# Performance work log

Hardware: AMD Instinct MI355X
Metric: run time of the kernel (lower is better)

Reference implementation:

```python
import jax, jax.numpy as jnp
import numpy as np

B, C, IH, IW = 16, 512, 28, 28
HEADS, DIM_HEAD = 8, 32
INNER = HEADS * DIM_HEAD            # 256
HIDDEN = 4 * C                      # 2048
N = IH * IW                         # 784 tokens
EPS = 1e-5


def _relative_index(ih, iw):
    coords = np.stack(np.meshgrid(np.arange(ih), np.arange(iw), indexing='ij')).reshape(2, -1)
    rel = coords[:, :, None] - coords[:, None, :]
    rel[0] += ih - 1
    rel[1] += iw - 1
    rel[0] *= 2 * iw - 1
    return jnp.asarray((rel[0] + rel[1]).reshape(-1))  # (n*n,)

REL_IDX = _relative_index(IH, IW)


def _layernorm(x, g, b):
    mu = jnp.mean(x, axis=-1, keepdims=True)
    var = jnp.mean(jnp.square(x - mu), axis=-1, keepdims=True)
    return (x - mu) * jax.lax.rsqrt(var + EPS) * g + b


def setup_inputs() -> dict:
    key = jax.random.key(0)
    ks = jax.random.split(key, 12)
    s = lambda fan_in: 1.0 / np.sqrt(fan_in)
    return {
        'x': jax.random.normal(ks[0], (B, C, IH, IW), jnp.float32),
        'ln1_g': jnp.ones((C,), jnp.float32),
        'ln1_b': jnp.zeros((C,), jnp.float32),
        'qkv_w': jax.random.normal(ks[1], (C, 3 * INNER), jnp.float32) * s(C),
        'qkv_b': jnp.zeros((3 * INNER,), jnp.float32),
        'out_w': jax.random.normal(ks[2], (INNER, C), jnp.float32) * s(INNER),
        'out_b': jnp.zeros((C,), jnp.float32),
        'rel_table': jax.random.normal(ks[3], ((2 * IH - 1) * (2 * IW - 1), HEADS), jnp.float32) * 0.02,
        'ln2_g': jnp.ones((C,), jnp.float32),
        'ln2_b': jnp.zeros((C,), jnp.float32),
        'ff_w1': jax.random.normal(ks[4], (C, HIDDEN), jnp.float32) * s(C),
        'ff_b1': jnp.zeros((HIDDEN,), jnp.float32),
        'ff_w2': jax.random.normal(ks[5], (HIDDEN, C), jnp.float32) * s(HIDDEN),
        'ff_b2': jnp.zeros((C,), jnp.float32),
    }


def reference(x, ln1_g, ln1_b, qkv_w, qkv_b, out_w, out_b, rel_table,
              ln2_g, ln2_b, ff_w1, ff_b1, ff_w2, ff_b2):
    scale = DIM_HEAD ** -0.5
    # b c h w -> b n c
    xs = x.reshape(B, C, N).transpose(0, 2, 1)

    # --- PreNorm attention branch ---
    h = _layernorm(xs, ln1_g, ln1_b)
    qkv = h @ qkv_w + qkv_b                               # [B, N, 3*INNER]
    q, k, v = jnp.split(qkv, 3, axis=-1)
    split_heads = lambda t: t.reshape(B, N, HEADS, DIM_HEAD).transpose(0, 2, 1, 3)
    q, k, v = map(split_heads, (q, k, v))                 # [B, H, N, d]
    dots = jnp.einsum('bhnd,bhmd->bhnm', q, k) * scale    # [B, H, N, N]
    bias = rel_table[REL_IDX].reshape(N, N, HEADS).transpose(2, 0, 1)  # [H, N, N]
    attn = jax.nn.softmax(dots + bias[None], axis=-1)
    o = jnp.einsum('bhnm,bhmd->bhnd', attn, v)            # [B, H, N, d]
    o = o.transpose(0, 2, 1, 3).reshape(B, N, INNER)
    o = o @ out_w + out_b                                 # [B, N, C]
    xs = xs + o                                           # residual

    # --- PreNorm FFN branch ---
    h = _layernorm(xs, ln2_g, ln2_b)
    h = jax.nn.gelu(h @ ff_w1 + ff_b1, approximate=False)
    h = h @ ff_w2 + ff_b2
    xs = xs + h

    # b n c -> b c h w
    return xs.transpose(0, 2, 1).reshape(B, C, IH, IW)
```

## Files before the change

kernel.cpp:

```cpp
#include <hip/hip_runtime.h>
#include <hip/hip_bf16.h>

#define DEVI __device__ __forceinline__

typedef __attribute__((ext_vector_type(8))) short bf16x8;
typedef __attribute__((ext_vector_type(4))) float f32x4;
typedef __attribute__((ext_vector_type(4))) unsigned u32x4;

static constexpr int BB = 16, CC = 512, NT = 784, HD = 8, DH = 32;
static constexpr int INNER = 256, HID = 2048, MTOT = BB * NT;

DEVI short f2bf(float x) {
  unsigned u = __builtin_bit_cast(unsigned, x);
  u += 0x7fffu + ((u >> 16) & 1u);
  return (short)(u >> 16);
}

DEVI void gll16(const void* g, void* l) {
  __builtin_amdgcn_global_load_lds(
      (const __attribute__((address_space(1))) unsigned int*)g,
      (__attribute__((address_space(3))) unsigned int*)l, 16, 0, 0);
}

__device__ void wprep_body(const float* __restrict__ W, short* __restrict__ WT,
                           int K0, int N0, int bx, int by, float* smem) {
  float (*tile)[33] = (float(*)[33])smem;
  const int tk0 = bx * 32, tn0 = by * 32;
  const int tx = threadIdx.x & 31, ty = threadIdx.x >> 5;
#pragma unroll
  for (int i = 0; i < 4; ++i)
    tile[ty + i * 8][tx] = W[(size_t)(tk0 + ty + i * 8) * N0 + tn0 + tx];
  __syncthreads();
#pragma unroll
  for (int i = 0; i < 4; ++i)
    WT[(size_t)(tn0 + ty + i * 8) * K0 + tk0 + tx] = f2bf(tile[tx][ty + i * 8]);
}

__global__ void prep_kernel(const float* __restrict__ qkv_w, short* __restrict__ wqkvT,
                            const float* __restrict__ out_w, short* __restrict__ woutT,
                            const float* __restrict__ ff_w1, short* __restrict__ wf1T,
                            const float* __restrict__ ff_w2, short* __restrict__ wf2T,
                            const float* __restrict__ x, float* __restrict__ xs,
                            const float* __restrict__ rel, short* __restrict__ bt) {
  __shared__ float smem[64 * 17];
  const int bid = blockIdx.x;
  if (bid < 384) {
    wprep_body(qkv_w, wqkvT, 512, 768, bid & 15, bid >> 4, smem);
  } else if (bid < 512) {
    int l = bid - 384;
    wprep_body(out_w, woutT, 256, 512, l & 7, l >> 3, smem);
  } else if (bid < 1536) {
    int l = bid - 512;
    wprep_body(ff_w1, wf1T, 512, 2048, l & 15, l >> 4, smem);
  } else if (bid < 2560) {
    int l = bid - 1536;
    wprep_body(ff_w2, wf2T, 2048, 512, l & 63, l >> 6, smem);
  } else if (bid < 8832) {
    int l = bid - 2560;
    float (*tile)[17] = (float(*)[17])smem;
    const int n0 = (l % 49) * 16, c0 = ((l / 49) & 7) * 64, b = l / 392;
    const int tx = threadIdx.x & 15, ty = threadIdx.x >> 4;
    const float* p = x + ((size_t)b * CC + c0) * NT + n0;
#pragma unroll
    for (int i = 0; i < 4; ++i)
      tile[ty + i * 16][tx] = p[(size_t)(ty + i * 16) * NT + tx];
    __syncthreads();
    float* qd = xs + ((size_t)b * NT + n0) * CC + c0;
    const int cx = threadIdx.x & 63, ny = threadIdx.x >> 6;
#pragma unroll
    for (int i = 0; i < 4; ++i)
      qd[(size_t)(ny + i * 4) * CC + cx] = tile[cx][ny + i * 4];
  } else {
    int id = (bid - 8832) * 256 + threadIdx.x;
    int r = id & 3;
    int mr = (id >> 2) & 1;
    int lane = (id >> 3) & 63;
    int wid = (id >> 9) & 3;
    int t = id >> 11;
    int jhi = t % 49;
    int t2 = t / 49;
    int qc = t2 % 7;
    int h = t2 / 7;
    int i = qc * 128 + wid * 32 + mr * 16 + (lane >> 4) * 4 + r;
    if (i > 783) i = 783;
    int j = jhi * 16 + (lane & 15);
    int hi_ = i / 28, wi_ = i - hi_ * 28;
    int hj = j / 28, wj = j - hj * 28;
    int ridx = (hi_ - hj + 27) * 55 + (wi_ - wj + 27);
    bt[id] = f2bf(rel[ridx * 8 + h] * 1.4426950408889634f);
  }
}

__global__ void ln_kernel(const float* __restrict__ in, const float* __restrict__ gw,
                          const float* __restrict__ bw, short* __restrict__ h_out) {
  int t = blockIdx.x;
  int tid = threadIdx.x;
  const float* p = in + (size_t)t * CC;
  float v0 = p[tid], v1 = p[tid + 256];
  float s = v0 + v1, s2 = v0 * v0 + v1 * v1;
#pragma unroll
  for (int m = 1; m < 64; m <<= 1) {
    s += __shfl_xor(s, m);
    s2 += __shfl_xor(s2, m);
  }
  __shared__ float red[8];
  int wid = tid >> 6;
  if ((tid & 63) == 0) { red[wid] = s; red[4 + wid] = s2; }
  __syncthreads();
  s = red[0] + red[1] + red[2] + red[3];
  s2 = red[4] + red[5] + red[6] + red[7];
  float mu = s * (1.f / 512.f);
  float var = s2 * (1.f / 512.f) - mu * mu;
  float rs = rsqrtf(var + 1e-5f);
  h_out[(size_t)t * CC + tid] = f2bf((v0 - mu) * rs * gw[tid] + bw[tid]);
  h_out[(size_t)t * CC + tid + 256] = f2bf((v1 - mu) * rs * gw[tid + 256] + bw[tid + 256]);
}

template <int EPI, int BM, int BN, int MINW>
__global__ __launch_bounds__(256, MINW) void gemm_bt(
    const short* __restrict__ A, const short* __restrict__ BT,
    const float* __restrict__ bias, int K, void* __restrict__ out0,
    void* __restrict__ o1, void* __restrict__ o2, const float* __restrict__ res,
    int Nld, int nn) {
  __shared__ short As[BM * 64];
  __shared__ short Bs[BN * 64];
  const int tid = threadIdx.x;
  const int lane = tid & 63, wid = tid >> 6;
  const int nwg = gridDim.x, orig = blockIdx.x;
  const int q = nwg >> 3, rm = nwg & 7;
  const int xcd = orig & 7, idx = orig >> 3;
  const int wg = (xcd < rm) ? (xcd * (q + 1) + idx)
                            : (rm * (q + 1) + (xcd - rm) * q + idx);
  const int mt = wg / nn, nt = wg - mt * nn;
  const int m0 = mt * BM, n0 = nt * BN;
  const int wm = wid >> 1, wn = wid & 1;
  constexpr int MF = BM >> 5;
  constexpr int NF = BN >> 5;
  constexpr int ACALLS = BM / 32;
  constexpr int BCALLS = BN / 32;
  const int lg = lane >> 4, ln = lane & 15;

  f32x4 acc[MF][NF] = {};
  for (int kt = 0; kt < K; kt += 64) {
#pragma unroll
    for (int call = 0; call < ACALLS; ++call) {
      int cb = call * 256 + (wid << 6);
      int c = cb + lane;
      int row = c >> 3, j8 = c & 7;
      gll16(A + (size_t)(m0 + row) * K + kt + (j8 ^ (row & 7)) * 8, &As[cb * 8]);
    }
#pragma unroll
    for (int call = 0; call < BCALLS; ++call) {
      int cb = call * 256 + (wid << 6);
      int c = cb + lane;
      int row = c >> 3, j8 = c & 7;
      gll16(BT + (size_t)(n0 + row) * K + kt + (j8 ^ (row & 7)) * 8, &Bs[cb * 8]);
    }
    __syncthreads();
#pragma unroll
    for (int kk = 0; kk < 64; kk += 32) {
      bf16x8 af[MF], bfr[NF];
#pragma unroll
      for (int mf = 0; mf < MF; ++mf) {
        int r = wm * (BM >> 1) + mf * 16 + ln;
        af[mf] = *(const bf16x8*)&As[r * 64 + ((((kk >> 3) + lg) ^ (r & 7)) << 3)];
      }
#pragma unroll
      for (int nf = 0; nf < NF; ++nf) {
        int r = wn * (BN >> 1) + nf * 16 + ln;
        bfr[nf] = *(const bf16x8*)&Bs[r * 64 + ((((kk >> 3) + lg) ^ (r & 7)) << 3)];
      }
#pragma unroll
      for (int mf = 0; mf < MF; ++mf)
#pragma unroll
        for (int nf = 0; nf < NF; ++nf)
          acc[mf][nf] = __builtin_amdgcn_mfma_f32_16x16x32_bf16(af[mf], bfr[nf], acc[mf][nf], 0, 0, 0);
    }
    __syncthreads();
  }
#pragma unroll
  for (int mf = 0; mf < MF; ++mf)
#pragma unroll
    for (int nf = 0; nf < NF; ++nf) {
      int col = n0 + wn * (BN >> 1) + nf * 16 + ln;
      float bv = bias[col];
#pragma unroll
      for (int r = 0; r < 4; ++r) {
        int row = m0 + wm * (BM >> 1) + mf * 16 + lg * 4 + r;
        float val = acc[mf][nf][r] + bv;
        if (EPI == 0) {
          int which = col >> 8, head = (col >> 5) & 7, dd = col & 31;
          int b = row / NT, n = row - b * NT;
          if (which == 2) {
            ((short*)o2)[((size_t)((b * HD + head) * DH + dd)) * NT + n] = f2bf(val);
          } else {
            short* dst = (which == 0) ? (short*)out0 : (short*)o1;
            dst[((size_t)((b * HD + head) * NT + n)) * DH + dd] = f2bf(val);
          }
        } else if (EPI == 1) {
          ((float*)out0)[(size_t)row * Nld + col] = val + res[(size_t)row * Nld + col];
        } else if (EPI == 2) {
          float v2 = val * val;
          float y = val * fmaf(0.102944458f, v2, 2.30225813f);
          y = fminf(y, 80.f);
          float e = __builtin_amdgcn_exp2f(y);
          float gl = val * e * __builtin_amdgcn_rcpf(e + 1.0f);
          ((short*)out0)[(size_t)row * Nld + col] = f2bf(gl);
        } else {
          int b = row / NT, n = row - b * NT;
          ((float*)out0)[((size_t)(b * CC + col)) * NT + n] =
              val + res[(size_t)row * Nld + col];
        }
      }
    }
}

__global__ __launch_bounds__(256, 3) void attn_kernel(
    const short* __restrict__ qb, const short* __restrict__ kb,
    const short* __restrict__ vtg, const short* __restrict__ bt,
    short* __restrict__ ob) {
  const int qc = blockIdx.x;
  const int bh = blockIdx.y;
  const int b = bh >> 3, h = bh & 7;
  const int tid = threadIdx.x, lane = tid & 63, wid = tid >> 6;
  const int qbase = qc * 128;
  const int lg = lane >> 4, ln = lane & 15;
  const float SC2 = 0.17677669529663687f * 1.4426950408889634f;

  __shared__ short Pl[4][32 * 136];
  short* pw = Pl[wid];

  const short* qrow = qb + (size_t)bh * NT * DH;
  bf16x8 aq[2];
#pragma unroll
  for (int mr = 0; mr < 2; ++mr) {
    int r = qbase + wid * 32 + mr * 16 + ln;
    if (r > 783) r = 783;
    aq[mr] = *(const bf16x8*)(qrow + (size_t)r * DH + lg * 8);
  }
  float l_run[2][4] = {};
  f32x4 o_acc[2][2] = {};
  const short* kbase = kb + (size_t)bh * NT * DH;
  const short* vbase = vtg + (size_t)bh * DH * NT;
  const short* btw = bt + ((size_t)(h * 7 + qc) * 49) * 2048 + wid * 512 + lane * 8;

  bf16x8 kcur[8];
#pragma unroll
  for (int nf = 0; nf < 8; ++nf)
    kcur[nf] = *(const bf16x8*)(kbase + (size_t)(nf * 16 + ln) * DH + lg * 8);

  for (int jt = 0; jt < 768; jt += 128) {
    const int jt0 = jt >> 4;
    bf16x8 knext[8];
#pragma unroll
    for (int nf = 0; nf < 8; ++nf) {
      int j = jt + 128 + nf * 16 + ln;
      if (j > 783) j = 783;
      knext[nf] = *(const bf16x8*)(kbase + (size_t)j * DH + lg * 8);
    }
    bf16x8 vreg[4][2];
#pragma unroll
    for (int kk = 0; kk < 4; ++kk)
#pragma unroll
      for (int dr = 0; dr < 2; ++dr)
        vreg[kk][dr] = *(const bf16x8*)(vbase + (size_t)(dr * 16 + ln) * NT + jt + kk * 32 + lg * 8);

#pragma unroll
    for (int nf = 0; nf < 8; ++nf) {
      const u32x4 bq = *(const u32x4*)(btw + (size_t)(jt0 + nf) * 2048);
#pragma unroll
      for (int mr = 0; mr < 2; ++mr) {
        f32x4 zr = {0.f, 0.f, 0.f, 0.f};
        f32x4 s = __builtin_amdgcn_mfma_f32_16x16x32_bf16(aq[mr], kcur[nf], zr, 0, 0, 0);
        unsigned w0 = mr ? bq.z : bq.x, w1 = mr ? bq.w : bq.y;
        float p0 = __builtin_amdgcn_exp2f(fmaf(s[0], SC2, __builtin_bit_cast(float, w0 << 16)));
        float p1 = __builtin_amdgcn_exp2f(fmaf(s[1], SC2, __builtin_bit_cast(float, w0 & 0xffff0000u)));
        float p2 = __builtin_amdgcn_exp2f(fmaf(s[2], SC2, __builtin_bit_cast(float, w1 << 16)));
        float p3 = __builtin_amdgcn_exp2f(fmaf(s[3], SC2, __builtin_bit_cast(float, w1 & 0xffff0000u)));
        l_run[mr][0] += p0;
        l_run[mr][1] += p1;
        l_run[mr][2] += p2;
        l_run[mr][3] += p3;
        int pa = (mr * 16 + lg * 4) * 136 + nf * 16 + ln;
        pw[pa] = f2bf(p0);
        pw[pa + 136] = f2bf(p1);
        pw[pa + 272] = f2bf(p2);
        pw[pa + 408] = f2bf(p3);
      }
    }
#pragma unroll
    for (int kk = 0; kk < 4; ++kk) {
      bf16x8 ap[2];
#pragma unroll
      for (int mr = 0; mr < 2; ++mr)
        ap[mr] = *(const bf16x8*)&pw[(mr * 16 + ln) * 136 + kk * 32 + lg * 8];
#pragma unroll
      for (int mr = 0; mr < 2; ++mr)
#pragma unroll
        for (int dr = 0; dr < 2; ++dr)
          o_acc[mr][dr] = __builtin_amdgcn_mfma_f32_16x16x32_bf16(ap[mr], vreg[kk][dr], o_acc[mr][dr], 0, 0, 0);
    }
#pragma unroll
    for (int nf = 0; nf < 8; ++nf) kcur[nf] = knext[nf];
  }

  {
#pragma unroll
    for (int mr = 0; mr < 2; ++mr) {
      int pa = (mr * 16 + lg * 4) * 136 + 16 + ln;
#pragma unroll
      for (int r = 0; r < 4; ++r) pw[pa + r * 136] = 0;
    }
    const u32x4 bq = *(const u32x4*)(btw + (size_t)48 * 2048);
#pragma unroll
    for (int mr = 0; mr < 2; ++mr) {
      f32x4 zr = {0.f, 0.f, 0.f, 0.f};
      f32x4 s = __builtin_amdgcn_mfma_f32_16x16x32_bf16(aq[mr], kcur[0], zr, 0, 0, 0);
      unsigned w0 = mr ? bq.z : bq.x, w1 = mr ? bq.w : bq.y;
      float p0 = __builtin_amdgcn_exp2f(fmaf(s[0], SC2, __builtin_bit_cast(float, w0 << 16)));
      float p1 = __builtin_amdgcn_exp2f(fmaf(s[1], SC2, __builtin_bit_cast(float, w0 & 0xffff0000u)));
      float p2 = __builtin_amdgcn_exp2f(fmaf(s[2], SC2, __builtin_bit_cast(float, w1 << 16)));
      float p3 = __builtin_amdgcn_exp2f(fmaf(s[3], SC2, __builtin_bit_cast(float, w1 & 0xffff0000u)));
      l_run[mr][0] += p0;
      l_run[mr][1] += p1;
      l_run[mr][2] += p2;
      l_run[mr][3] += p3;
      int pa = (mr * 16 + lg * 4) * 136 + ln;
      pw[pa] = f2bf(p0);
      pw[pa + 136] = f2bf(p1);
      pw[pa + 272] = f2bf(p2);
      pw[pa + 408] = f2bf(p3);
    }
    {
      bf16x8 ap[2], bv[2];
#pragma unroll
      for (int mr = 0; mr < 2; ++mr)
        ap[mr] = *(const bf16x8*)&pw[(mr * 16 + ln) * 136 + lg * 8];
#pragma unroll
      for (int dr = 0; dr < 2; ++dr) {
        int col = 768 + lg * 8;
        if (col < NT)
          bv[dr] = *(const bf16x8*)(vbase + (size_t)(dr * 16 + ln) * NT + col);
        else {
          bf16x8 zz = {};
          bv[dr] = zz;
        }
      }
#pragma unroll
      for (int mr = 0; mr < 2; ++mr)
#pragma unroll
        for (int dr = 0; dr < 2; ++dr)
          o_acc[mr][dr] = __builtin_amdgcn_mfma_f32_16x16x32_bf16(ap[mr], bv[dr], o_acc[mr][dr], 0, 0, 0);
    }
  }

#pragma unroll
  for (int msk = 1; msk < 16; msk <<= 1)
#pragma unroll
    for (int mr = 0; mr < 2; ++mr)
#pragma unroll
      for (int r = 0; r < 4; ++r) l_run[mr][r] += __shfl_xor(l_run[mr][r], msk);

#pragma unroll
  for (int mr = 0; mr < 2; ++mr) {
    float rinv[4];
#pragma unroll
    for (int r = 0; r < 4; ++r) rinv[r] = 1.0f / l_run[mr][r];
#pragma unroll
    for (int dr = 0; dr < 2; ++dr)
#pragma unroll
      for (int r = 0; r < 4; ++r) {
        int row = qbase + wid * 32 + mr * 16 + lg * 4 + r;
        if (row < 784) {
          float val = o_acc[mr][dr][r] * rinv[r];
          ob[((size_t)(b * NT + row)) * INNER + h * DH + dr * 16 + ln] = f2bf(val);
        }
      }
  }
}

extern "C" void kernel_launch(void* const* d_in, const int* in_sizes, int n_in,
                              void* d_out, int out_size, void* d_ws, size_t ws_size,
                              hipStream_t stream) {
  const float* x = (const float*)d_in[0];
  const float* ln1_g = (const float*)d_in[1];
  const float* ln1_b = (const float*)d_in[2];
  const float* qkv_w = (const float*)d_in[3];
  const float* qkv_b = (const float*)d_in[4];
  const float* out_w = (const float*)d_in[5];
  const float* out_b = (const float*)d_in[6];
  const float* rel_table = (const float*)d_in[7];
  const float* ln2_g = (const float*)d_in[8];
  const float* ln2_b = (const float*)d_in[9];
  const float* ff_w1 = (const float*)d_in[10];
  const float* ff_b1 = (const float*)d_in[11];
  const float* ff_w2 = (const float*)d_in[12];
  const float* ff_b2 = (const float*)d_in[13];
  float* out = (float*)d_out;
  char* ws = (char*)d_ws;

  constexpr size_t OFF_XS = 0;
  constexpr size_t OFF_H = 25690112;
  constexpr size_t OFF_WQKV = 38535168;
  constexpr size_t OFF_WOUT = 39321600;
  constexpr size_t OFF_WF1 = 39583744;
  constexpr size_t OFF_WF2 = 41680896;
  constexpr size_t OFF_Q = 43778048;
  constexpr size_t OFF_K = 50200576;
  constexpr size_t OFF_VT = 63045632;
  constexpr size_t OFF_O = 69468160;
  constexpr size_t OFF_XS2 = 75890688;
  constexpr size_t OFF_G = 101580800;

  float* xs = (float*)(ws + OFF_XS);
  short* h = (short*)(ws + OFF_H);
  short* wqkvT = (short*)(ws + OFF_WQKV);
  short* woutT = (short*)(ws + OFF_WOUT);
  short* wf1T = (short*)(ws + OFF_WF1);
  short* wf2T = (short*)(ws + OFF_WF2);
  short* qb = (short*)(ws + OFF_Q);
  short* kb = (short*)(ws + OFF_K);
  short* vt = (short*)(ws + OFF_VT);
  short* ob = (short*)(ws + OFF_O);
  short* bt = (short*)(ws + OFF_XS2);
  float* xs2 = (float*)(ws + OFF_XS2);
  short* g = (short*)(ws + OFF_G);

  prep_kernel<<<30784, 256, 0, stream>>>(qkv_w, wqkvT, out_w, woutT,
                                         ff_w1, wf1T, ff_w2, wf2T,
                                         x, xs, rel_table, bt);

  ln_kernel<<<MTOT, 256, 0, stream>>>(xs, ln1_g, ln1_b, h);

  gemm_bt<0, 128, 64, 3><<<1176, 256, 0, stream>>>(h, wqkvT, qkv_b, 512, qb, kb, vt, nullptr, 0, 12);

  attn_kernel<<<dim3(7, 128), 256, 0, stream>>>(qb, kb, vt, bt, ob);

  gemm_bt<1, 128, 64, 3><<<784, 256, 0, stream>>>(ob, woutT, out_b, 256, xs2, nullptr, nullptr, xs, 512, 8);

  ln_kernel<<<MTOT, 256, 0, stream>>>(xs2, ln2_g, ln2_b, h);

  gemm_bt<2, 128, 128, 3><<<1568, 256, 0, stream>>>(h, wf1T, ff_b1, 512, g, nullptr, nullptr, nullptr, 2048, 16);

  gemm_bt<3, 64, 64, 3><<<1568, 256, 0, stream>>>(g, wf2T, ff_b2, 2048, out, nullptr, nullptr, xs2, 512, 8);
}
```

Baseline: 225.2 us.

## Shrink attention query tile to 64 rows and enlarge FFN2 GEMM tile

Each attention wave now handles 16 query rows instead of 32, so a block covers 64 queries and the grid grows from 7 to 13 query chunks per head. The bias-table layout written by the prep kernel is re-indexed to match, and the prep grid shrinks accordingly. The aim is more blocks and lower register pressure for better occupancy, paid for by reloading each K/V tile for twice as many blocks. Separately, the last FFN GEMM switches from a 64x64 to a 128x64 tile with half the blocks.

```diff
diff --git a/kernel.cpp b/kernel.cpp
--- a/kernel.cpp
+++ b/kernel.cpp
@@ -5,7 +5,7 @@
 
 typedef __attribute__((ext_vector_type(8))) short bf16x8;
 typedef __attribute__((ext_vector_type(4))) float f32x4;
-typedef __attribute__((ext_vector_type(4))) unsigned u32x4;
+typedef __attribute__((ext_vector_type(2))) unsigned u32x2;
 
 static constexpr int BB = 16, CC = 512, NT = 784, HD = 8, DH = 32;
 static constexpr int INNER = 256, HID = 2048, MTOT = BB * NT;
@@ -73,15 +73,14 @@
   } else {
     int id = (bid - 8832) * 256 + threadIdx.x;
     int r = id & 3;
-    int mr = (id >> 2) & 1;
-    int lane = (id >> 3) & 63;
-    int wid = (id >> 9) & 3;
-    int t = id >> 11;
+    int lane = (id >> 2) & 63;
+    int wid = (id >> 8) & 3;
+    int t = id >> 10;
     int jhi = t % 49;
     int t2 = t / 49;
-    int qc = t2 % 7;
-    int h = t2 / 7;
-    int i = qc * 128 + wid * 32 + mr * 16 + (lane >> 4) * 4 + r;
+    int qc = t2 % 13;
+    int h = t2 / 13;
+    int i = qc * 64 + wid * 16 + ((lane >> 4) << 2) + r;
     if (i > 783) i = 783;
     int j = jhi * 16 + (lane & 15);
     int hi_ = i / 28, wi_ = i - hi_ * 28;
@@ -223,26 +222,25 @@
   const int bh = blockIdx.y;
   const int b = bh >> 3, h = bh & 7;
   const int tid = threadIdx.x, lane = tid & 63, wid = tid >> 6;
-  const int qbase = qc * 128;
   const int lg = lane >> 4, ln = lane & 15;
+  const int rb = qc * 64 + wid * 16;
   const float SC2 = 0.17677669529663687f * 1.4426950408889634f;
 
-  __shared__ short Pl[4][32 * 136];
+  __shared__ short Pl[4][16 * 136];
   short* pw = Pl[wid];
 
   const short* qrow = qb + (size_t)bh * NT * DH;
-  bf16x8 aq[2];
-#pragma unroll
-  for (int mr = 0; mr < 2; ++mr) {
-    int r = qbase + wid * 32 + mr * 16 + ln;
+  bf16x8 aq;
+  {
+    int r = rb + ln;
     if (r > 783) r = 783;
-    aq[mr] = *(const bf16x8*)(qrow + (size_t)r * DH + lg * 8);
-  }
-  float l_run[2][4] = {};
-  f32x4 o_acc[2][2] = {};
+    aq = *(const bf16x8*)(qrow + (size_t)r * DH + lg * 8);
+  }
+  float l_run[4] = {};
+  f32x4 o_acc[2] = {};
   const short* kbase = kb + (size_t)bh * NT * DH;
   const short* vbase = vtg + (size_t)bh * DH * NT;
-  const short* btw = bt + ((size_t)(h * 7 + qc) * 49) * 2048 + wid * 512 + lane * 8;
+  const short* btw = bt + ((size_t)(h * 13 + qc) * 49) * 1024 + wid * 256 + lane * 4;
 
   bf16x8 kcur[8];
 #pragma unroll
@@ -267,75 +265,61 @@
 
 #pragma unroll
     for (int nf = 0; nf < 8; ++nf) {
-      const u32x4 bq = *(const u32x4*)(btw + (size_t)(jt0 + nf) * 2048);
-#pragma unroll
-      for (int mr = 0; mr < 2; ++mr) {
-        f32x4 zr = {0.f, 0.f, 0.f, 0.f};
-        f32x4 s = __builtin_amdgcn_mfma_f32_16x16x32_bf16(aq[mr], kcur[nf], zr, 0, 0, 0);
-        unsigned w0 = mr ? bq.z : bq.x, w1 = mr ? bq.w : bq.y;
-        float p0 = __builtin_amdgcn_exp2f(fmaf(s[0], SC2, __builtin_bit_cast(float, w0 << 16)));
-        float p1 = __builtin_amdgcn_exp2f(fmaf(s[1], SC2, __builtin_bit_cast(float, w0 & 0xffff0000u)));
-        float p2 = __builtin_amdgcn_exp2f(fmaf(s[2], SC2, __builtin_bit_cast(float, w1 << 16)));
-        float p3 = __builtin_amdgcn_exp2f(fmaf(s[3], SC2, __builtin_bit_cast(float, w1 & 0xffff0000u)));
-        l_run[mr][0] += p0;
-        l_run[mr][1] += p1;
-        l_run[mr][2] += p2;
-        l_run[mr][3] += p3;
-        int pa = (mr * 16 + lg * 4) * 136 + nf * 16 + ln;
-        pw[pa] = f2bf(p0);
-        pw[pa + 136] = f2bf(p1);
-        pw[pa + 272] = f2bf(p2);
-        pw[pa + 408] = f2bf(p3);
-      }
-    }
-#pragma unroll
-    for (int kk = 0; kk < 4; ++kk) {
-      bf16x8 ap[2];
-#pragma unroll
-      for (int mr = 0; mr < 2; ++mr)
-        ap[mr] = *(const bf16x8*)&pw[(mr * 16 + ln) * 136 + kk * 32 + lg * 8];
-#pragma unroll
-      for (int mr = 0; mr < 2; ++mr)
-#pragma unroll
-        for (int dr = 0; dr < 2; ++dr)
-          o_acc[mr][dr] = __builtin_amdgcn_mfma_f32_16x16x32_bf16(ap[mr], vreg[kk][dr], o_acc[mr][dr], 0, 0, 0);
-    }
-#pragma unroll
-    for (int nf = 0; nf < 8; ++nf) kcur[nf] = knext[nf];
-  }
-
-  {
-#pragma unroll
-    for (int mr = 0; mr < 2; ++mr) {
-      int pa = (mr * 16 + lg * 4) * 136 + 16 + ln;
-#pragma unroll
-      for (int r = 0; r < 4; ++r) pw[pa + r * 136] = 0;
-    }
-    const u32x4 bq = *(const u32x4*)(btw + (size_t)48 * 2048);
-#pragma unroll
-    for (int mr = 0; mr < 2; ++mr) {
+      const u32x2 bq = *(const u32x2*)(btw + (size_t)(jt0 + nf) * 1024);
       f32x4 zr = {0.f, 0.f, 0.f, 0.f};
-      f32x4 s = __builtin_amdgcn_mfma_f32_16x16x32_bf16(aq[mr], kcur[0], zr, 0, 0, 0);
-      unsigned w0 = mr ? bq.z : bq.x, w1 = mr ? bq.w : bq.y;
+      f32x4 s = __builtin_amdgcn_mfma_f32_16x16x32_bf16(aq, kcur[nf], zr, 0, 0, 0);
+      unsigned w0 = bq.x, w1 = bq.y;
       float p0 = __builtin_amdgcn_exp2f(fmaf(s[0], SC2, __builtin_bit_cast(float, w0 << 16)));
       float p1 = __builtin_amdgcn_exp2f(fmaf(s[1], SC2, __builtin_bit_cast(float, w0 & 0xffff0000u)));
       float p2 = __builtin_amdgcn_exp2f(fmaf(s[2], SC2, __builtin_bit_cast(float, w1 << 16)));
       float p3 = __builtin_amdgcn_exp2f(fmaf(s[3], SC2, __builtin_bit_cast(float, w1 & 0xffff0000u)));
-      l_run[mr][0] += p0;
-      l_run[mr][1] += p1;
-      l_run[mr][2] += p2;
-      l_run[mr][3] += p3;
-      int pa = (mr * 16 + lg * 4) * 136 + ln;
+      l_run[0] += p0;
+      l_run[1] += p1;
+      l_run[2] += p2;
+      l_run[3] += p3;
+      int pa = (lg * 4) * 136 + nf * 16 + ln;
       pw[pa] = f2bf(p0);
       pw[pa + 136] = f2bf(p1);
       pw[pa + 272] = f2bf(p2);
       pw[pa + 408] = f2bf(p3);
     }
+#pragma unroll
+    for (int kk = 0; kk < 4; ++kk) {
+      bf16x8 ap = *(const bf16x8*)&pw[ln * 136 + kk * 32 + lg * 8];
+#pragma unroll
+      for (int dr = 0; dr < 2; ++dr)
+        o_acc[dr] = __builtin_amdgcn_mfma_f32_16x16x32_bf16(ap, vreg[kk][dr], o_acc[dr], 0, 0, 0);
+    }
+#pragma unroll
+    for (int nf = 0; nf < 8; ++nf) kcur[nf] = knext[nf];
+  }
+
+  {
     {
-      bf16x8 ap[2], bv[2];
-#pragma unroll
-      for (int mr = 0; mr < 2; ++mr)
-        ap[mr] = *(const bf16x8*)&pw[(mr * 16 + ln) * 136 + lg * 8];
+      int pa = (lg * 4) * 136 + 16 + ln;
+#pragma unroll
+      for (int r = 0; r < 4; ++r) pw[pa + r * 136] = 0;
+    }
+    const u32x2 bq = *(const u32x2*)(btw + (size_t)48 * 1024);
+    f32x4 zr = {0.f, 0.f, 0.f, 0.f};
+    f32x4 s = __builtin_amdgcn_mfma_f32_16x16x32_bf16(aq, kcur[0], zr, 0, 0, 0);
+    unsigned w0 = bq.x, w1 = bq.y;
+    float p0 = __builtin_amdgcn_exp2f(fmaf(s[0], SC2, __builtin_bit_cast(float, w0 << 16)));
+    float p1 = __builtin_amdgcn_exp2f(fmaf(s[1], SC2, __builtin_bit_cast(float, w0 & 0xffff0000u)));
+    float p2 = __builtin_amdgcn_exp2f(fmaf(s[2], SC2, __builtin_bit_cast(float, w1 << 16)));
+    float p3 = __builtin_amdgcn_exp2f(fmaf(s[3], SC2, __builtin_bit_cast(float, w1 & 0xffff0000u)));
+    l_run[0] += p0;
+    l_run[1] += p1;
+    l_run[2] += p2;
+    l_run[3] += p3;
+    int pa = (lg * 4) * 136 + ln;
+    pw[pa] = f2bf(p0);
+    pw[pa + 136] = f2bf(p1);
+    pw[pa + 272] = f2bf(p2);
+    pw[pa + 408] = f2bf(p3);
+    {
+      bf16x8 ap = *(const bf16x8*)&pw[ln * 136 + lg * 8];
+      bf16x8 bv[2];
 #pragma unroll
       for (int dr = 0; dr < 2; ++dr) {
         int col = 768 + lg * 8;
@@ -347,36 +331,29 @@
         }
       }
 #pragma unroll
-      for (int mr = 0; mr < 2; ++mr)
-#pragma unroll
-        for (int dr = 0; dr < 2; ++dr)
-          o_acc[mr][dr] = __builtin_amdgcn_mfma_f32_16x16x32_bf16(ap[mr], bv[dr], o_acc[mr][dr], 0, 0, 0);
+      for (int dr = 0; dr < 2; ++dr)
+        o_acc[dr] = __builtin_amdgcn_mfma_f32_16x16x32_bf16(ap, bv[dr], o_acc[dr], 0, 0, 0);
     }
   }
 
 #pragma unroll
   for (int msk = 1; msk < 16; msk <<= 1)
 #pragma unroll
-    for (int mr = 0; mr < 2; ++mr)
-#pragma unroll
-      for (int r = 0; r < 4; ++r) l_run[mr][r] += __shfl_xor(l_run[mr][r], msk);
-
-#pragma unroll
-  for (int mr = 0; mr < 2; ++mr) {
-    float rinv[4];
-#pragma unroll
-    for (int r = 0; r < 4; ++r) rinv[r] = 1.0f / l_run[mr][r];
-#pragma unroll
-    for (int dr = 0; dr < 2; ++dr)
-#pragma unroll
-      for (int r = 0; r < 4; ++r) {
-        int row = qbase + wid * 32 + mr * 16 + lg * 4 + r;
-        if (row < 784) {
-          float val = o_acc[mr][dr][r] * rinv[r];
-          ob[((size_t)(b * NT + row)) * INNER + h * DH + dr * 16 + ln] = f2bf(val);
-        }
+    for (int r = 0; r < 4; ++r) l_run[r] += __shfl_xor(l_run[r], msk);
+
+  float rinv[4];
+#pragma unroll
+  for (int r = 0; r < 4; ++r) rinv[r] = 1.0f / l_run[r];
+#pragma unroll
+  for (int dr = 0; dr < 2; ++dr)
+#pragma unroll
+    for (int r = 0; r < 4; ++r) {
+      int row = rb + lg * 4 + r;
+      if (row < 784) {
+        float val = o_acc[dr][r] * rinv[r];
+        ob[((size_t)(b * NT + row)) * INNER + h * DH + dr * 16 + ln] = f2bf(val);
       }
-  }
+    }
 }
 
 extern "C" void kernel_launch(void* const* d_in, const int* in_sizes, int n_in,
@@ -426,7 +403,7 @@
   float* xs2 = (float*)(ws + OFF_XS2);
   short* g = (short*)(ws + OFF_G);
 
-  prep_kernel<<<30784, 256, 0, stream>>>(qkv_w, wqkvT, out_w, woutT,
+  prep_kernel<<<29216, 256, 0, stream>>>(qkv_w, wqkvT, out_w, woutT,
                                          ff_w1, wf1T, ff_w2, wf2T,
                                          x, xs, rel_table, bt);
 
@@ -434,7 +411,7 @@
 
   gemm_bt<0, 128, 64, 3><<<1176, 256, 0, stream>>>(h, wqkvT, qkv_b, 512, qb, kb, vt, nullptr, 0, 12);
 
-  attn_kernel<<<dim3(7, 128), 256, 0, stream>>>(qb, kb, vt, bt, ob);
+  attn_kernel<<<dim3(13, 128), 256, 0, stream>>>(qb, kb, vt, bt, ob);
 
   gemm_bt<1, 128, 64, 3><<<784, 256, 0, stream>>>(ob, woutT, out_b, 256, xs2, nullptr, nullptr, xs, 512, 8);
 
@@ -442,5 +419,5 @@
 
   gemm_bt<2, 128, 128, 3><<<1568, 256, 0, stream>>>(h, wf1T, ff_b1, 512, g, nullptr, nullptr, nullptr, 2048, 16);
 
-  gemm_bt<3, 64, 64, 3><<<1568, 256, 0, stream>>>(g, wf2T, ff_b2, 2048, out, nullptr, nullptr, xs2, 512, 8);
-}
+  gemm_bt<3, 128, 64, 3><<<784, 256, 0, stream>>>(g, wf2T, ff_b2, 2048, out, nullptr, nullptr, xs2, 512, 8);
+}
```

Result: no change. 223.3 us (-0.9%).
